# Kernel optimization log

Hardware: AMD Instinct MI355X
Metric: run time of the kernel (lower is better)

## Reference

```python
import jax, jax.numpy as jnp
import numpy as np

SMOOTH_STEP_PARAM = 1.0  # = 1/gamma in the TEL paper
DEPTH = 6


def smooth_step(x):
    # TEL smooth-step: 0 for u<=-1/2, 1 for u>=1/2, cubic -2u^3+1.5u+0.5 inside.
    u = SMOOTH_STEP_PARAM * x
    inner = (-2.0 * u + 1.5) * u * u + (u + 0.5) * 0.0 + (-2.0 * u ** 3 + 1.5 * u + 0.5)
    # use single clean expression for the cubic
    cubic = -2.0 * u ** 3 + 1.5 * u + 0.5
    return jnp.where(u <= -0.5, 0.0, jnp.where(u >= 0.5, 1.0, cubic))


def setup_inputs() -> dict:
    key = jax.random.key(0)
    k1, k2, k3 = jax.random.split(key, 3)
    B, D, T, O = 32768, 1024, 8, 128
    num_leaves = 2 ** DEPTH
    x = jax.random.normal(k1, (B, D), dtype=jnp.float32)
    # RandomUniform(-0.01, 0.01) initializers in the original layer
    node_weights = jax.random.uniform(k2, (T, D, num_leaves - 1), dtype=jnp.float32,
                                      minval=-0.01, maxval=0.01)
    leaf_weights = jax.random.uniform(k3, (T, O, num_leaves), dtype=jnp.float32,
                                      minval=-0.01, maxval=0.01)
    return {"x": x, "node_weights": node_weights, "leaf_weights": leaf_weights}


def reference(x, node_weights, leaf_weights):
    B = x.shape[0]
    T = node_weights.shape[0]
    # routing probabilities at every internal node (BFS order): [B, T, 2^depth-1]
    s = smooth_step(jnp.einsum('bd,tdi->bti', x, node_weights))
    # accumulate leaf reach probabilities level by level (left child gets s)
    mu = jnp.ones((B, T, 1), dtype=x.dtype)
    start = 0
    for level in range(DEPTH):
        width = 2 ** level
        s_lvl = s[:, :, start:start + width]           # [B, T, width]
        mu = jnp.stack([mu * s_lvl, mu * (1.0 - s_lvl)], axis=-1)
        mu = mu.reshape(B, T, 2 * width)
        start += width
    # weighted sum of leaf vectors, summed over trees (sum_outputs=True)
    return jnp.einsum('btl,tol->bo', mu, leaf_weights)
```

## Files before the change

### kernel.cpp

```cpp
#include <hip/hip_runtime.h>
#include <hip/hip_bf16.h>
#include <stdint.h>

#define KDIM 1024
#define TSTR 72
#define RSTR 576

typedef __attribute__((ext_vector_type(4))) float f32x4;
typedef __attribute__((ext_vector_type(8))) short bf16x8;

#define WS_LB_OFF ((size_t)1 << 20)

__device__ __forceinline__ unsigned short f2bf_rne(float f) {
    unsigned u = __float_as_uint(f);
    u = (u + 0x7fffu + ((u >> 16) & 1u)) >> 16;
    return (unsigned short)u;
}

__device__ __forceinline__ unsigned int pack2_bf16(float a, float b) {
    __hip_bfloat162 h = __float22bfloat162_rn(make_float2(a, b));
    union { __hip_bfloat162 h; unsigned int u; } cv;
    cv.h = h;
    return cv.u;
}

__device__ __forceinline__ float gs_get(const uint4* q, int i) {
    uint4 v = q[i >> 3];
    int c = (i >> 1) & 3;
    unsigned w = (c == 0) ? v.x : (c == 1) ? v.y : (c == 2) ? v.z : v.w;
    return __uint_as_float((i & 1) ? (w & 0xffff0000u) : (w << 16));
}

__global__ void prep_w(const float* __restrict__ nw, unsigned short* __restrict__ wb) {
    int idx = blockIdx.x * 256 + threadIdx.x;
    int kl = idx & 31;
    int n  = (idx >> 5) & 511;
    int ks = idx >> 14;
    int cp = kl >> 3, e = kl & 7;
    int kchunk = cp ^ (n & 3);
    int d = ks * 32 + kchunk * 8 + e;
    int t = n >> 6, i = n & 63;
    float v = (i < 63) ? nw[(t * KDIM + d) * 63 + i] : 0.0f;
    wb[idx] = f2bf_rne(v);
}

__global__ void prep_l(const float* __restrict__ lw, unsigned short* __restrict__ lb) {
    int idx = blockIdx.x * 256 + threadIdx.x;
    int kk = idx & 31;
    int o  = (idx >> 5) & 127;
    int kq = idx >> 12;
    int c = kq * 32 + kk;
    int t = c >> 6, l = c & 63;
    lb[idx] = f2bf_rne(lw[(t * 128 + o) * 64 + l]);
}

__launch_bounds__(256, 2)
__global__ void fused(const float* __restrict__ x, const unsigned short* __restrict__ wb,
                      const unsigned short* __restrict__ lb, float* __restrict__ out) {
    __shared__ union __align__(16) {
        struct {
            unsigned short xs[64 * 40];
            unsigned short wl[512 * 32];
        } k;
        unsigned short st[32 * RSTR];
    } sm;

    const int tid  = threadIdx.x;
    const int wave = tid >> 6, lane = tid & 63;
    const int quad = lane >> 4, l16 = lane & 15;
    const int mb   = blockIdx.x;

    f32x4 acc[8][4];
    const f32x4 z4 = {0.f, 0.f, 0.f, 0.f};
    #pragma unroll
    for (int a = 0; a < 8; ++a)
        #pragma unroll
        for (int b = 0; b < 4; ++b) acc[a][b] = z4;

    const int xrow = tid >> 2, xq = tid & 3;
    const float* xg0 = x + (size_t)(mb * 64 + xrow) * KDIM + xq * 8;

    for (int ks = 0; ks < 32; ++ks) {
        __syncthreads();
        const unsigned short* wks = wb + (size_t)ks * (512 * 32);
        #pragma unroll
        for (int it = 0; it < 8; ++it) {
            const unsigned short* gp = wks + (size_t)(it * 256 + tid) * 8;
            __builtin_amdgcn_global_load_lds(
                (const __attribute__((address_space(1))) unsigned int*)gp,
                (__attribute__((address_space(3))) unsigned int*)&sm.k.wl[(it * 256 + wave * 64) * 8],
                16, 0, 0);
        }
        {
            const float4* xg = (const float4*)(xg0 + ks * 32);
            float4 f0 = xg[0], f1 = xg[1];
            uint4 p;
            p.x = pack2_bf16(f0.x, f0.y); p.y = pack2_bf16(f0.z, f0.w);
            p.z = pack2_bf16(f1.x, f1.y); p.w = pack2_bf16(f1.z, f1.w);
            *(uint4*)&sm.k.xs[xrow * 40 + xq * 8] = p;
        }
        __syncthreads();
        bf16x8 af[8], bf[4];
        #pragma unroll
        for (int ct = 0; ct < 8; ++ct) {
            int col = wave * 128 + ct * 16 + l16;
            int chunk = quad ^ (col & 3);
            af[ct] = *(const bf16x8*)&sm.k.wl[col * 32 + chunk * 8];
        }
        #pragma unroll
        for (int rt = 0; rt < 4; ++rt)
            bf[rt] = *(const bf16x8*)&sm.k.xs[(rt * 16 + l16) * 40 + quad * 8];
        #pragma unroll
        for (int ct = 0; ct < 8; ++ct)
            #pragma unroll
            for (int rt = 0; rt < 4; ++rt)
                acc[ct][rt] = __builtin_amdgcn_mfma_f32_16x16x32_bf16(af[ct], bf[rt], acc[ct][rt], 0, 0, 0);
    }

    #pragma unroll
    for (int p = 0; p < 2; ++p) {
        __syncthreads();
        #pragma unroll
        for (int rt2 = 0; rt2 < 2; ++rt2) {
            int rowl = rt2 * 16 + l16;
            #pragma unroll
            for (int ct = 0; ct < 8; ++ct) {
                int colb = wave * 128 + ct * 16 + quad * 4;
                f32x4 a = acc[ct][p * 2 + rt2];
                float s0[4];
                #pragma unroll
                for (int j = 0; j < 4; ++j) {
                    float u = a[j];
                    u = fminf(fmaxf(u, -0.5f), 0.5f);
                    s0[j] = u * (1.5f - 2.0f * u * u) + 0.5f;
                }
                uint2 pk;
                pk.x = pack2_bf16(s0[0], s0[1]);
                pk.y = pack2_bf16(s0[2], s0[3]);
                *(uint2*)&sm.st[rowl * RSTR + (colb >> 6) * TSTR + (colb & 63)] = pk;
            }
        }
        __syncthreads();
        {
            int r = tid >> 3, t = tid & 7;
            unsigned short* base = &sm.st[r * RSTR + t * TSTR];
            uint4 q[8];
            #pragma unroll
            for (int c = 0; c < 8; ++c) q[c] = *(const uint4*)(base + c * 8);
            float mu[32];
            mu[0] = 1.0f;
            int start = 0;
            #pragma unroll
            for (int lvl = 0; lvl < 5; ++lvl) {
                int width = 1 << lvl;
                #pragma unroll
                for (int j = width - 1; j >= 0; --j) {
                    float m = mu[j], s_ = gs_get(q, start + j);
                    mu[2 * j + 1] = m * (1.0f - s_);
                    mu[2 * j]     = m * s_;
                }
                start += width;
            }
            #pragma unroll
            for (int c = 0; c < 8; ++c) {
                unsigned pk2[4];
                #pragma unroll
                for (int e = 0; e < 4; ++e) {
                    int j = c * 4 + e;
                    float m = mu[j], s_ = gs_get(q, 31 + j);
                    pk2[e] = pack2_bf16(m * s_, m * (1.0f - s_));
                }
                uint4 v; v.x = pk2[0]; v.y = pk2[1]; v.z = pk2[2]; v.w = pk2[3];
                *(uint4*)(base + c * 8) = v;
            }
        }
        __syncthreads();
        {
            int rtile = wave & 1, ob = (wave >> 1) * 64;
            f32x4 a2[4];
            a2[0] = z4; a2[1] = z4; a2[2] = z4; a2[3] = z4;
            #pragma unroll
            for (int kq = 0; kq < 16; ++kq) {
                int c0 = kq * 32 + quad * 8;
                bf16x8 bmu = *(const bf16x8*)&sm.st[(rtile * 16 + l16) * RSTR + (c0 >> 6) * TSTR + (c0 & 63)];
                #pragma unroll
                for (int ct = 0; ct < 4; ++ct) {
                    int o = ob + ct * 16 + l16;
                    bf16x8 alf = *(const bf16x8*)(lb + (size_t)(kq * 128 + o) * 32 + quad * 8);
                    a2[ct] = __builtin_amdgcn_mfma_f32_16x16x32_bf16(alf, bmu, a2[ct], 0, 0, 0);
                }
            }
            #pragma unroll
            for (int ct = 0; ct < 4; ++ct) {
                int rowg = mb * 64 + p * 32 + rtile * 16 + l16;
                int og = ob + ct * 16 + quad * 4;
                *(f32x4*)(out + (size_t)rowg * 128 + og) = a2[ct];
            }
        }
    }
}

extern "C" void kernel_launch(void* const* d_in, const int* in_sizes, int n_in,
                              void* d_out, int out_size, void* d_ws, size_t ws_size,
                              hipStream_t stream) {
    const float* x  = (const float*)d_in[0];
    const float* nw = (const float*)d_in[1];
    const float* lw = (const float*)d_in[2];
    float* out = (float*)d_out;

    unsigned short* wb = (unsigned short*)d_ws;
    unsigned short* lb = (unsigned short*)((char*)d_ws + WS_LB_OFF);

    prep_w<<<2048, 256, 0, stream>>>(nw, wb);
    prep_l<<<256, 256, 0, stream>>>(lw, lb);
    fused<<<512, 256, 0, stream>>>(x, wb, lb, out);
}
```

Measured before the change: 240.5 us.

## Load MFMA fragments directly from global, dropping LDS staging in main loop

The weight and leaf prep kernels now write bf16 data already arranged in per-lane MFMA fragment order. The main GEMM loop loads A and B fragments straight from global memory into registers, converting x to bf16 in registers. This removes the LDS staging buffers and both __syncthreads per K step. In exchange each wave issues its own global loads with no cross-wave sharing through LDS, which raises L2/global traffic and leaves load latency to be hidden by occupancy alone.

```diff
diff --git a/kernel.cpp b/kernel.cpp
--- a/kernel.cpp
+++ b/kernel.cpp
@@ -31,25 +31,36 @@
     return __uint_as_float((i & 1) ? (w & 0xffff0000u) : (w << 16));
 }
 
+__device__ __forceinline__ bf16x8 cvt8(f32x4 lo, f32x4 hi) {
+    union { uint4 u; bf16x8 v; } cv;
+    cv.u.x = pack2_bf16(lo[0], lo[1]);
+    cv.u.y = pack2_bf16(lo[2], lo[3]);
+    cv.u.z = pack2_bf16(hi[0], hi[1]);
+    cv.u.w = pack2_bf16(hi[2], hi[3]);
+    return cv.v;
+}
+
 __global__ void prep_w(const float* __restrict__ nw, unsigned short* __restrict__ wb) {
     int idx = blockIdx.x * 256 + threadIdx.x;
-    int kl = idx & 31;
-    int n  = (idx >> 5) & 511;
-    int ks = idx >> 14;
-    int cp = kl >> 3, e = kl & 7;
-    int kchunk = cp ^ (n & 3);
-    int d = ks * 32 + kchunk * 8 + e;
-    int t = n >> 6, i = n & 63;
-    float v = (i < 63) ? nw[(t * KDIM + d) * 63 + i] : 0.0f;
+    int e    = idx & 7;
+    int lane = (idx >> 3) & 63;
+    int cb   = (idx >> 9) & 31;
+    int ks   = idx >> 14;
+    int col = cb * 16 + (lane & 15);
+    int k   = ks * 32 + (lane >> 4) * 8 + e;
+    int t = col >> 6, i = col & 63;
+    float v = (i < 63) ? nw[(t * KDIM + k) * 63 + i] : 0.0f;
     wb[idx] = f2bf_rne(v);
 }
 
 __global__ void prep_l(const float* __restrict__ lw, unsigned short* __restrict__ lb) {
     int idx = blockIdx.x * 256 + threadIdx.x;
-    int kk = idx & 31;
-    int o  = (idx >> 5) & 127;
-    int kq = idx >> 12;
-    int c = kq * 32 + kk;
+    int e    = idx & 7;
+    int lane = (idx >> 3) & 63;
+    int obk  = (idx >> 9) & 7;
+    int kq   = idx >> 12;
+    int o = obk * 16 + (lane & 15);
+    int c = kq * 32 + (lane >> 4) * 8 + e;
     int t = c >> 6, l = c & 63;
     lb[idx] = f2bf_rne(lw[(t * 128 + o) * 64 + l]);
 }
@@ -57,13 +68,7 @@
 __launch_bounds__(256, 2)
 __global__ void fused(const float* __restrict__ x, const unsigned short* __restrict__ wb,
                       const unsigned short* __restrict__ lb, float* __restrict__ out) {
-    __shared__ union __align__(16) {
-        struct {
-            unsigned short xs[64 * 40];
-            unsigned short wl[512 * 32];
-        } k;
-        unsigned short st[32 * RSTR];
-    } sm;
+    __shared__ __align__(16) unsigned short st[32 * RSTR];
 
     const int tid  = threadIdx.x;
     const int wave = tid >> 6, lane = tid & 63;
@@ -77,39 +82,29 @@
         #pragma unroll
         for (int b = 0; b < 4; ++b) acc[a][b] = z4;
 
-    const int xrow = tid >> 2, xq = tid & 3;
-    const float* xg0 = x + (size_t)(mb * 64 + xrow) * KDIM + xq * 8;
+    const float* xr0 = x + (size_t)(mb * 64 + 0 * 16 + l16) * KDIM + quad * 8;
+    const float* xr1 = x + (size_t)(mb * 64 + 1 * 16 + l16) * KDIM + quad * 8;
+    const float* xr2 = x + (size_t)(mb * 64 + 2 * 16 + l16) * KDIM + quad * 8;
+    const float* xr3 = x + (size_t)(mb * 64 + 3 * 16 + l16) * KDIM + quad * 8;
+    const unsigned short* wb0 = wb + (size_t)(wave * 8 * 64 + lane) * 8;
 
     for (int ks = 0; ks < 32; ++ks) {
-        __syncthreads();
-        const unsigned short* wks = wb + (size_t)ks * (512 * 32);
-        #pragma unroll
-        for (int it = 0; it < 8; ++it) {
-            const unsigned short* gp = wks + (size_t)(it * 256 + tid) * 8;
-            __builtin_amdgcn_global_load_lds(
-                (const __attribute__((address_space(1))) unsigned int*)gp,
-                (__attribute__((address_space(3))) unsigned int*)&sm.k.wl[(it * 256 + wave * 64) * 8],
-                16, 0, 0);
-        }
+        bf16x8 af[8], bf[4];
         {
-            const float4* xg = (const float4*)(xg0 + ks * 32);
-            float4 f0 = xg[0], f1 = xg[1];
-            uint4 p;
-            p.x = pack2_bf16(f0.x, f0.y); p.y = pack2_bf16(f0.z, f0.w);
-            p.z = pack2_bf16(f1.x, f1.y); p.w = pack2_bf16(f1.z, f1.w);
-            *(uint4*)&sm.k.xs[xrow * 40 + xq * 8] = p;
-        }
-        __syncthreads();
-        bf16x8 af[8], bf[4];
-        #pragma unroll
-        for (int ct = 0; ct < 8; ++ct) {
-            int col = wave * 128 + ct * 16 + l16;
-            int chunk = quad ^ (col & 3);
-            af[ct] = *(const bf16x8*)&sm.k.wl[col * 32 + chunk * 8];
-        }
-        #pragma unroll
-        for (int rt = 0; rt < 4; ++rt)
-            bf[rt] = *(const bf16x8*)&sm.k.xs[(rt * 16 + l16) * 40 + quad * 8];
+            f32x4 lo, hi;
+            lo = *(const f32x4*)(xr0 + ks * 32); hi = *(const f32x4*)(xr0 + ks * 32 + 4);
+            bf[0] = cvt8(lo, hi);
+            lo = *(const f32x4*)(xr1 + ks * 32); hi = *(const f32x4*)(xr1 + ks * 32 + 4);
+            bf[1] = cvt8(lo, hi);
+            lo = *(const f32x4*)(xr2 + ks * 32); hi = *(const f32x4*)(xr2 + ks * 32 + 4);
+            bf[2] = cvt8(lo, hi);
+            lo = *(const f32x4*)(xr3 + ks * 32); hi = *(const f32x4*)(xr3 + ks * 32 + 4);
+            bf[3] = cvt8(lo, hi);
+        }
+        const unsigned short* wbase = wb0 + (size_t)ks * 16384;
+        #pragma unroll
+        for (int ct = 0; ct < 8; ++ct)
+            af[ct] = *(const bf16x8*)(wbase + ct * 512);
         #pragma unroll
         for (int ct = 0; ct < 8; ++ct)
             #pragma unroll
@@ -137,13 +132,13 @@
                 uint2 pk;
                 pk.x = pack2_bf16(s0[0], s0[1]);
                 pk.y = pack2_bf16(s0[2], s0[3]);
-                *(uint2*)&sm.st[rowl * RSTR + (colb >> 6) * TSTR + (colb & 63)] = pk;
+                *(uint2*)&st[rowl * RSTR + (colb >> 6) * TSTR + (colb & 63)] = pk;
             }
         }
         __syncthreads();
         {
             int r = tid >> 3, t = tid & 7;
-            unsigned short* base = &sm.st[r * RSTR + t * TSTR];
+            unsigned short* base = &st[r * RSTR + t * TSTR];
             uint4 q[8];
             #pragma unroll
             for (int c = 0; c < 8; ++c) q[c] = *(const uint4*)(base + c * 8);
@@ -176,24 +171,24 @@
         }
         __syncthreads();
         {
-            int rtile = wave & 1, ob = (wave >> 1) * 64;
+            int rtile = wave & 1, obw = wave >> 1;
             f32x4 a2[4];
             a2[0] = z4; a2[1] = z4; a2[2] = z4; a2[3] = z4;
             #pragma unroll
             for (int kq = 0; kq < 16; ++kq) {
                 int c0 = kq * 32 + quad * 8;
-                bf16x8 bmu = *(const bf16x8*)&sm.st[(rtile * 16 + l16) * RSTR + (c0 >> 6) * TSTR + (c0 & 63)];
+                bf16x8 bmu = *(const bf16x8*)&st[(rtile * 16 + l16) * RSTR + (c0 >> 6) * TSTR + (c0 & 63)];
+                const unsigned short* lbase = lb + ((size_t)((kq * 8 + obw * 4) * 64 + lane)) * 8;
                 #pragma unroll
                 for (int ct = 0; ct < 4; ++ct) {
-                    int o = ob + ct * 16 + l16;
-                    bf16x8 alf = *(const bf16x8*)(lb + (size_t)(kq * 128 + o) * 32 + quad * 8);
+                    bf16x8 alf = *(const bf16x8*)(lbase + ct * 512);
                     a2[ct] = __builtin_amdgcn_mfma_f32_16x16x32_bf16(alf, bmu, a2[ct], 0, 0, 0);
                 }
             }
             #pragma unroll
             for (int ct = 0; ct < 4; ++ct) {
                 int rowg = mb * 64 + p * 32 + rtile * 16 + l16;
-                int og = ob + ct * 16 + quad * 4;
+                int og = obw * 64 + ct * 16 + quad * 4;
                 *(f32x4*)(out + (size_t)rowg * 128 + og) = a2[ct];
             }
         }
```

New measurement: 274.1 us. +13.9%, slower.
